# Kernel optimization log

Measured on AMD Instinct MI355X. Metric: run time of the kernel, lower is better.

## Reference

```python
import jax, jax.numpy as jnp
from jax import lax
import numpy as np

B, S = 128, 512
TARGET_SIZE = 32
T = TARGET_SIZE + 4  # tag_size, START = T-2, END = T-1


def setup_inputs() -> dict:
    key = jax.random.key(0)
    k1, k2, k3, k4 = jax.random.split(key, 4)
    feats = jax.random.normal(k1, (B, S, T), dtype=jnp.float32)
    # contiguous-prefix mask (lengths in [S//2, S])
    lengths = jax.random.randint(k2, (B,), S // 2, S + 1)
    mask = (jnp.arange(S)[None, :] < lengths[:, None]).astype(jnp.int32)
    tags = jax.random.randint(k3, (B, S), 0, TARGET_SIZE).astype(jnp.int32)
    # learned transitions, with the hard constraints from __init__
    transitions = 0.1 * jax.random.normal(k4, (T, T), dtype=jnp.float32)
    transitions = transitions.at[:, T - 2].set(-1000.0)  # nothing -> START
    transitions = transitions.at[T - 1, :].set(-1000.0)  # END -> nothing
    return {"feats": feats, "transitions": transitions, "mask": mask, "tags": tags}


def _nll(feats, transitions, mask, tags):
    # feats: (B,S,T), transitions: (T,T) with [i,j] = score(prev=i -> cur=j)
    b, s, t = feats.shape
    START, END = t - 2, t - 1
    fdtype = feats.dtype

    feats_t = jnp.swapaxes(feats, 0, 1)   # (S,B,T)
    mask_t = jnp.swapaxes(mask, 0, 1)     # (S,B)

    # ---- forward algorithm (partition function) ----
    # scores[t,b,i,j] = feats[b,t,j] + transitions[i,j]
    part0 = feats_t[0] + transitions[START][None, :]  # (B,T): alpha after step 0

    def step(part, xs):
        f_step, m_step = xs  # (B,T), (B,)
        # cur[b,i,j] = feats[b,j] + trans[i,j] + part[b,i]
        cur = f_step[:, None, :] + transitions[None, :, :] + part[:, :, None]
        new_part = jax.nn.logsumexp(cur, axis=1)  # (B,T)
        part = jnp.where(m_step[:, None].astype(bool), new_part, part)
        return part, None

    part, _ = lax.scan(step, part0, (feats_t[1:], mask_t[1:]))
    final = jax.nn.logsumexp(part[:, :, None] + transitions[None, :, :], axis=1)  # (B,T)
    forward_score = jnp.sum(final[:, END])

    # ---- gold score ----
    tags_i = tags.astype(jnp.int32)
    prev_tags = jnp.concatenate(
        [jnp.full((b, 1), START, dtype=jnp.int32), tags_i[:, :-1]], axis=1)  # (B,S)
    emit = jnp.take_along_axis(feats, tags_i[:, :, None], axis=2)[:, :, 0]    # (B,S)
    trans_sc = transitions[prev_tags, tags_i]                                  # (B,S)
    tg_energy = jnp.sum((emit + trans_sc) * mask.astype(fdtype))
    lengths = jnp.sum(mask, axis=1).astype(jnp.int32)                          # (B,)
    end_ids = jnp.take_along_axis(tags_i, (lengths - 1)[:, None], axis=1)[:, 0]
    end_energy = jnp.sum(transitions[end_ids, END])
    gold_score = tg_energy + end_energy

    # average_batch = True
    return (forward_score - gold_score) / jnp.asarray(b, fdtype)


def reference(feats, transitions, mask, tags):
    return _nll(feats, transitions, mask, tags)
```

## Files before the change

kernel.cpp:

```cpp
#include <hip/hip_runtime.h>


namespace {
constexpr int kB = 128;
constexpr int kS = 512;
constexpr int kT = 36;
constexpr int kStart = 34;
constexpr int kEnd = 35;

__device__ float g_vec[kB * 8][64];
__device__ float g_cc[kB * 8];

__device__ __forceinline__ float readlane_f(float v, int lane) {
    return __builtin_bit_cast(float, __builtin_amdgcn_readlane(__builtin_bit_cast(int, v), lane));
}

__device__ __forceinline__ float wave_sum(float v) {
#pragma unroll
    for (int off = 32; off; off >>= 1) v += __shfl_xor(v, off, 64);
    return v;
}
__device__ __forceinline__ int wave_sum_i(int v) {
#pragma unroll
    for (int off = 32; off; off >>= 1) v += __shfl_xor(v, off, 64);
    return v;
}

#define FOR34(X) \
    X(0, 0) X(1, 1) X(2, 2) X(3, 3) X(4, 0) X(5, 1) X(6, 2) X(7, 3) \
    X(8, 0) X(9, 1) X(10, 2) X(11, 3) X(12, 0) X(13, 1) X(14, 2) X(15, 3) \
    X(16, 0) X(17, 1) X(18, 2) X(19, 3) X(20, 0) X(21, 1) X(22, 2) X(23, 3) \
    X(24, 0) X(25, 1) X(26, 2) X(27, 3) X(28, 0) X(29, 1) X(30, 2) X(31, 3) \
    X(32, 0) X(33, 1)

#define FMDECL(n, a) float Fm##n;
#define FMINIT(n, a) Fm##n = __expf(trans[(n)*kT + jc]);
#define BMDECL(n, a) float Bm##n;
#define BMINIT(n, a) Bm##n = __expf(trans[jc * kT + (n)]);
#define FDOT(n, a) v##a = fmaf(readlane_f(q, n), Fm##n, v##a);
#define BDOT(n, a) w##a = fmaf(readlane_f(pp, n), Bm##n, w##a);

#define LDT(t) fl[(size_t)(((t) < 0) ? 0 : (((t) > kS - 1) ? (kS - 1) : (t))) * kT]

__device__ __forceinline__ int seq_len(const int* mb, int j) {
    int len = 0;
#pragma unroll
    for (int k = 0; k < kS / 64; ++k) len += mb[k * 64 + j];
    return __builtin_amdgcn_readfirstlane(wave_sum_i(len));
}

__global__ __attribute__((amdgpu_flat_work_group_size(64, 64),
                          amdgpu_waves_per_eu(1, 1)))
void crf_chain_kernel(const float* __restrict__ feats,
                      const float* __restrict__ trans,
                      const int* __restrict__ mask) {
    const int b = blockIdx.x >> 3;
    const int wv = blockIdx.x & 7;
    const int j = threadIdx.x;
    const int jc = (j < kT) ? j : (kT - 1);
    const float* fbase = feats + (size_t)b * kS * kT;
    const float* fl = fbase + jc;
    const int* mb = mask + b * kS;

    const int len = seq_len(mb, j);
    const int c = (len + 3) / 5;
    const int Gp = (c + 3) >> 2;

    float C = 0.f;

    if (wv < 4) {
        FOR34(FMDECL)
        FOR34(FMINIT)
        const int t0 = 1 + wv * c;
        const int cnt = c;
        float q;
        if (wv == 0) {
            const float a0 = (j < kT) ? (fl[0] + trans[kStart * kT + jc]) : -1e30f;
            C = readlane_f(a0, 0);
            q = __expf(a0 - C);
        } else {
            q = (jc == kStart) ? 0.f : 1.f;
        }

        auto fstep = [&](float ef, int s) {
            float v0 = 0.f, v1 = 0.f, v2 = 0.f, v3 = 0.f;
            FOR34(FDOT)
            const float nq = ((v0 + v1) + (v2 + v3)) * ef;
            q = (s < cnt) ? nq : q;
        };

        float p0, p1, p2, p3, e0, e1, e2, e3;
        p0 = LDT(t0 + 0); p1 = LDT(t0 + 1); p2 = LDT(t0 + 2); p3 = LDT(t0 + 3);
        e0 = __expf(p0); e1 = __expf(p1); e2 = __expf(p2); e3 = __expf(p3);
        p0 = LDT(t0 + 4); p1 = LDT(t0 + 5); p2 = LDT(t0 + 6); p3 = LDT(t0 + 7);

#pragma unroll 1
        for (int g = 0; g < Gp; ++g) {
            const int s = 4 * g;
            fstep(e0, s); fstep(e1, s + 1); fstep(e2, s + 2); fstep(e3, s + 3);
            e0 = __expf(p0); e1 = __expf(p1); e2 = __expf(p2); e3 = __expf(p3);
            p0 = LDT(t0 + s + 8);  p1 = LDT(t0 + s + 9);
            p2 = LDT(t0 + s + 10); p3 = LDT(t0 + s + 11);
            if (s + 4 < cnt) {
                const float mf = readlane_f(q, 0);
                C += __logf(mf);
                e0 *= __builtin_amdgcn_rcpf(mf);
            }
        }
        g_vec[blockIdx.x][j] = q;
        if (j == 0) g_cc[blockIdx.x] = C;
    } else {
        FOR34(BMDECL)
        FOR34(BMINIT)
        const bool real = (wv == 7);
        const int tau0 = real ? (len - 1) : ((wv - 2) * c);
        const int cnt = real ? (len - 1 - 4 * c) : c;
        float gg = real ? __expf(trans[jc * kT + kEnd])
                        : ((jc == kEnd) ? 0.f : 1.f);

        auto bstep = [&](float eb, int s) {
            const float pp = eb * gg;
            float w0 = 0.f, w1 = 0.f, w2 = 0.f, w3 = 0.f;
            FOR34(BDOT)
            const float ng = (w0 + w1) + (w2 + w3);
            gg = (s < cnt) ? ng : gg;
        };

        float p0, p1, p2, p3, e0, e1, e2, e3;
        p0 = LDT(tau0 - 0); p1 = LDT(tau0 - 1); p2 = LDT(tau0 - 2); p3 = LDT(tau0 - 3);
        e0 = __expf(p0); e1 = __expf(p1); e2 = __expf(p2); e3 = __expf(p3);
        p0 = LDT(tau0 - 4); p1 = LDT(tau0 - 5); p2 = LDT(tau0 - 6); p3 = LDT(tau0 - 7);

#pragma unroll 1
        for (int g = 0; g < Gp; ++g) {
            const int s = 4 * g;
            bstep(e0, s); bstep(e1, s + 1); bstep(e2, s + 2); bstep(e3, s + 3);
            e0 = __expf(p0); e1 = __expf(p1); e2 = __expf(p2); e3 = __expf(p3);
            p0 = LDT(tau0 - s - 8);  p1 = LDT(tau0 - s - 9);
            p2 = LDT(tau0 - s - 10); p3 = LDT(tau0 - s - 11);
            if (s + 4 < cnt) {
                const float mg = readlane_f(gg, 0);
                C += __logf(mg);
                e0 *= __builtin_amdgcn_rcpf(mg);
            }
        }
        g_vec[blockIdx.x][j] = gg;
        if (j == 0) g_cc[blockIdx.x] = C;
    }
}

__global__ __attribute__((amdgpu_flat_work_group_size(64, 64)))
void crf_meet_kernel(const float* __restrict__ feats,
                     const float* __restrict__ trans,
                     const int* __restrict__ mask,
                     const int* __restrict__ tags,
                     float* __restrict__ out) {
    const int b = blockIdx.x;
    const int j = threadIdx.x;
    const float* fbase = feats + (size_t)b * kS * kT;
    const int* mb = mask + b * kS;
    const int* tb = tags + b * kS;
    const int len = seq_len(mb, j);
    const int base = b * 8;

    const float msk = (j < kT) ? 1.f : 0.f;
    const float d1 = wave_sum(msk * g_vec[base + 4][j] * g_vec[base + 0][j]);
    const float d2 = wave_sum(msk * g_vec[base + 5][j] * g_vec[base + 1][j]);
    const float d3 = wave_sum(msk * g_vec[base + 6][j] * g_vec[base + 2][j]);
    const float d4 = wave_sum(msk * g_vec[base + 7][j] * g_vec[base + 3][j]);
    const float n1 = wave_sum(msk * g_vec[base + 1][j]);
    const float n2 = wave_sum(msk * g_vec[base + 2][j]);
    const float n3 = wave_sum(msk * g_vec[base + 3][j]);
    const float forward_b = g_cc[base + 0] + g_cc[base + 4] + g_cc[base + 5]
        + g_cc[base + 6] + g_cc[base + 7]
        + __logf(d1) + __logf(d2) + __logf(d3) + __logf(d4)
        - __logf(n1) - __logf(n2) - __logf(n3);

    float gold = 0.f;
    for (int k = j; k < kS; k += 64) {
        if (k < len) {
            const int tg = tb[k];
            const int pv = (k == 0) ? kStart : tb[k - 1];
            gold += fbase[(size_t)k * kT + tg] + trans[pv * kT + tg];
        }
    }
    gold = wave_sum(gold);

    if (j == 0) {
        gold += trans[tb[len - 1] * kT + kEnd];
        atomicAdd(out, (forward_b - gold) * (1.0f / kB));
    }
}

}

extern "C" void kernel_launch(void* const* d_in, const int* in_sizes, int n_in,
                              void* d_out, int out_size, void* d_ws, size_t ws_size,
                              hipStream_t stream) {
    const float* feats = (const float*)d_in[0];
    const float* trans = (const float*)d_in[1];
    const int* mask = (const int*)d_in[2];
    const int* tags = (const int*)d_in[3];
    float* out = (float*)d_out;

    (void)hipMemsetAsync(out, 0, sizeof(float), stream);
    crf_chain_kernel<<<dim3(kB * 8), dim3(64), 0, stream>>>(feats, trans, mask);
    crf_meet_kernel<<<dim3(kB), dim3(64), 0, stream>>>(feats, trans, mask, tags, out);
}
```

Baseline: 93.88 us.

## Use packed fp16 FMAs for the CRF transition matvec with per-step renormalization

The 34-term per-step matvec in both forward and backward chains is replaced by 17 packed fp16 v_pk_fma_f16 ops on lane pairs built with a DPP shift. To stay within fp16 range, the scaling is renormalized every step instead of every four, emissions are prescaled by 1/16 and a log correction is added afterward. The forward recurrence is reordered so the emission multiplies before the matvec. This roughly halves the FMA count on the serial critical path, but adds precision risk from fp16 accumulation plus extra readlane, log and rcp work on each step.

```diff
diff --git a/kernel.cpp b/kernel.cpp
--- a/kernel.cpp
+++ b/kernel.cpp
@@ -7,12 +7,26 @@
 constexpr int kT = 36;
 constexpr int kStart = 34;
 constexpr int kEnd = 35;
+constexpr float kPre = 0.0625f;
+constexpr float kCorr = 2.772588722f;
+
+typedef _Float16 h2 __attribute__((ext_vector_type(2)));
 
 __device__ float g_vec[kB * 8][64];
 __device__ float g_cc[kB * 8];
 
 __device__ __forceinline__ float readlane_f(float v, int lane) {
     return __builtin_bit_cast(float, __builtin_amdgcn_readlane(__builtin_bit_cast(int, v), lane));
+}
+__device__ __forceinline__ h2 readlane_h2(h2 v, int lane) {
+    return __builtin_bit_cast(h2, __builtin_amdgcn_readlane(__builtin_bit_cast(int, v), lane));
+}
+__device__ __forceinline__ h2 pk(float lo, float hi) {
+    return __builtin_bit_cast(h2, __builtin_amdgcn_cvt_pkrtz(lo, hi));
+}
+__device__ __forceinline__ float shl1_f(float x) {
+    const int xi = __builtin_bit_cast(int, x);
+    return __builtin_bit_cast(float, __builtin_amdgcn_update_dpp(0, xi, 0x101, 0xF, 0xF, true));
 }
 
 __device__ __forceinline__ float wave_sum(float v) {
@@ -26,19 +40,17 @@
     return v;
 }
 
-#define FOR34(X) \
+#define FOR17(X) \
     X(0, 0) X(1, 1) X(2, 2) X(3, 3) X(4, 0) X(5, 1) X(6, 2) X(7, 3) \
     X(8, 0) X(9, 1) X(10, 2) X(11, 3) X(12, 0) X(13, 1) X(14, 2) X(15, 3) \
-    X(16, 0) X(17, 1) X(18, 2) X(19, 3) X(20, 0) X(21, 1) X(22, 2) X(23, 3) \
-    X(24, 0) X(25, 1) X(26, 2) X(27, 3) X(28, 0) X(29, 1) X(30, 2) X(31, 3) \
-    X(32, 0) X(33, 1)
-
-#define FMDECL(n, a) float Fm##n;
-#define FMINIT(n, a) Fm##n = __expf(trans[(n)*kT + jc]);
-#define BMDECL(n, a) float Bm##n;
-#define BMINIT(n, a) Bm##n = __expf(trans[jc * kT + (n)]);
-#define FDOT(n, a) v##a = fmaf(readlane_f(q, n), Fm##n, v##a);
-#define BDOT(n, a) w##a = fmaf(readlane_f(pp, n), Bm##n, w##a);
+    X(16, 0)
+
+#define PKFDECL(k, a) h2 PF##k;
+#define PKFINIT(k, a) PF##k = pk(__expf(trans[(2 * (k)) * kT + jc]), __expf(trans[(2 * (k) + 1) * kT + jc]));
+#define PKBDECL(k, a) h2 PB##k;
+#define PKBINIT(k, a) PB##k = pk(__expf(trans[jc * kT + 2 * (k)]), __expf(trans[jc * kT + 2 * (k) + 1]));
+#define FD2(k, a) asm("v_pk_fma_f16 %0, %1, %2, %0" : "+v"(ac##a) : "v"(readlane_h2(pair, 2 * (k))), "v"(PF##k));
+#define BD2(k, a) asm("v_pk_fma_f16 %0, %1, %2, %0" : "+v"(ac##a) : "v"(readlane_h2(pair, 2 * (k))), "v"(PB##k));
 
 #define LDT(t) fl[(size_t)(((t) < 0) ? 0 : (((t) > kS - 1) ? (kS - 1) : (t))) * kT]
 
@@ -69,8 +81,8 @@
     float C = 0.f;
 
     if (wv < 4) {
-        FOR34(FMDECL)
-        FOR34(FMINIT)
+        FOR17(PKFDECL)
+        FOR17(PKFINIT)
         const int t0 = 1 + wv * c;
         const int cnt = c;
         float q;
@@ -83,35 +95,49 @@
         }
 
         auto fstep = [&](float ef, int s) {
-            float v0 = 0.f, v1 = 0.f, v2 = 0.f, v3 = 0.f;
-            FOR34(FDOT)
-            const float nq = ((v0 + v1) + (v2 + v3)) * ef;
+            const float z = q * ef;
+            const float zh = shl1_f(z);
+            const h2 pair = pk(z, zh);
+            h2 ac0 = __builtin_bit_cast(h2, 0), ac1 = __builtin_bit_cast(h2, 0);
+            h2 ac2 = __builtin_bit_cast(h2, 0), ac3 = __builtin_bit_cast(h2, 0);
+            FOR17(FD2)
+            const h2 sm = (ac0 + ac1) + (ac2 + ac3);
+            const float nq = (float)sm[0] + (float)sm[1];
             q = (s < cnt) ? nq : q;
         };
+        auto rnF = [&](float& e_next, int s_next) {
+            if (s_next < cnt) {
+                const float m = readlane_f(q, 0);
+                C += __logf(m);
+                e_next *= __builtin_amdgcn_rcpf(m);
+            }
+        };
 
         float p0, p1, p2, p3, e0, e1, e2, e3;
-        p0 = LDT(t0 + 0); p1 = LDT(t0 + 1); p2 = LDT(t0 + 2); p3 = LDT(t0 + 3);
-        e0 = __expf(p0); e1 = __expf(p1); e2 = __expf(p2); e3 = __expf(p3);
-        p0 = LDT(t0 + 4); p1 = LDT(t0 + 5); p2 = LDT(t0 + 6); p3 = LDT(t0 + 7);
+        p0 = 0.f;          p1 = LDT(t0);     p2 = LDT(t0 + 1); p3 = LDT(t0 + 2);
+        e0 = __expf(p0) * kPre; e1 = __expf(p1) * kPre;
+        e2 = __expf(p2) * kPre; e3 = __expf(p3) * kPre;
+        p0 = LDT(t0 + 3); p1 = LDT(t0 + 4); p2 = LDT(t0 + 5); p3 = LDT(t0 + 6);
 
 #pragma unroll 1
         for (int g = 0; g < Gp; ++g) {
             const int s = 4 * g;
-            fstep(e0, s); fstep(e1, s + 1); fstep(e2, s + 2); fstep(e3, s + 3);
-            e0 = __expf(p0); e1 = __expf(p1); e2 = __expf(p2); e3 = __expf(p3);
-            p0 = LDT(t0 + s + 8);  p1 = LDT(t0 + s + 9);
-            p2 = LDT(t0 + s + 10); p3 = LDT(t0 + s + 11);
-            if (s + 4 < cnt) {
-                const float mf = readlane_f(q, 0);
-                C += __logf(mf);
-                e0 *= __builtin_amdgcn_rcpf(mf);
-            }
-        }
+            fstep(e0, s);     rnF(e1, s + 1);
+            fstep(e1, s + 1); rnF(e2, s + 2);
+            fstep(e2, s + 2); rnF(e3, s + 3);
+            fstep(e3, s + 3);
+            e0 = __expf(p0) * kPre; e1 = __expf(p1) * kPre;
+            e2 = __expf(p2) * kPre; e3 = __expf(p3) * kPre;
+            p0 = LDT(t0 + s + 7);  p1 = LDT(t0 + s + 8);
+            p2 = LDT(t0 + s + 9);  p3 = LDT(t0 + s + 10);
+            rnF(e0, s + 4);
+        }
+        q *= __expf(LDT(t0 + cnt - 1));
         g_vec[blockIdx.x][j] = q;
-        if (j == 0) g_cc[blockIdx.x] = C;
+        if (j == 0) g_cc[blockIdx.x] = C + (float)cnt * kCorr;
     } else {
-        FOR34(BMDECL)
-        FOR34(BMINIT)
+        FOR17(PKBDECL)
+        FOR17(PKBINIT)
         const bool real = (wv == 7);
         const int tau0 = real ? (len - 1) : ((wv - 2) * c);
         const int cnt = real ? (len - 1 - 4 * c) : c;
@@ -119,33 +145,45 @@
                         : ((jc == kEnd) ? 0.f : 1.f);
 
         auto bstep = [&](float eb, int s) {
-            const float pp = eb * gg;
-            float w0 = 0.f, w1 = 0.f, w2 = 0.f, w3 = 0.f;
-            FOR34(BDOT)
-            const float ng = (w0 + w1) + (w2 + w3);
+            const float z = eb * gg;
+            const float zh = shl1_f(z);
+            const h2 pair = pk(z, zh);
+            h2 ac0 = __builtin_bit_cast(h2, 0), ac1 = __builtin_bit_cast(h2, 0);
+            h2 ac2 = __builtin_bit_cast(h2, 0), ac3 = __builtin_bit_cast(h2, 0);
+            FOR17(BD2)
+            const h2 sm = (ac0 + ac1) + (ac2 + ac3);
+            const float ng = (float)sm[0] + (float)sm[1];
             gg = (s < cnt) ? ng : gg;
+        };
+        auto rnB = [&](float& e_next, int s_next) {
+            if (s_next < cnt) {
+                const float m = readlane_f(gg, 0);
+                C += __logf(m);
+                e_next *= __builtin_amdgcn_rcpf(m);
+            }
         };
 
         float p0, p1, p2, p3, e0, e1, e2, e3;
         p0 = LDT(tau0 - 0); p1 = LDT(tau0 - 1); p2 = LDT(tau0 - 2); p3 = LDT(tau0 - 3);
-        e0 = __expf(p0); e1 = __expf(p1); e2 = __expf(p2); e3 = __expf(p3);
+        e0 = __expf(p0) * kPre; e1 = __expf(p1) * kPre;
+        e2 = __expf(p2) * kPre; e3 = __expf(p3) * kPre;
         p0 = LDT(tau0 - 4); p1 = LDT(tau0 - 5); p2 = LDT(tau0 - 6); p3 = LDT(tau0 - 7);
 
 #pragma unroll 1
         for (int g = 0; g < Gp; ++g) {
             const int s = 4 * g;
-            bstep(e0, s); bstep(e1, s + 1); bstep(e2, s + 2); bstep(e3, s + 3);
-            e0 = __expf(p0); e1 = __expf(p1); e2 = __expf(p2); e3 = __expf(p3);
+            bstep(e0, s);     rnB(e1, s + 1);
+            bstep(e1, s + 1); rnB(e2, s + 2);
+            bstep(e2, s + 2); rnB(e3, s + 3);
+            bstep(e3, s + 3);
+            e0 = __expf(p0) * kPre; e1 = __expf(p1) * kPre;
+            e2 = __expf(p2) * kPre; e3 = __expf(p3) * kPre;
             p0 = LDT(tau0 - s - 8);  p1 = LDT(tau0 - s - 9);
             p2 = LDT(tau0 - s - 10); p3 = LDT(tau0 - s - 11);
-            if (s + 4 < cnt) {
-                const float mg = readlane_f(gg, 0);
-                C += __logf(mg);
-                e0 *= __builtin_amdgcn_rcpf(mg);
-            }
+            rnB(e0, s + 4);
         }
         g_vec[blockIdx.x][j] = gg;
-        if (j == 0) g_cc[blockIdx.x] = C;
+        if (j == 0) g_cc[blockIdx.x] = C + (float)cnt * kCorr;
     }
 }
 
```

Result: slower. 105.3 us (+12.2%).
